# Performance work log

Measured on AMD Instinct MI355X. Metric: run time of the kernel, lower is better.

Reference implementation:

```python
import jax, jax.numpy as jnp
import numpy as np

B, T, E, H = 8, 2048, 1024, 64

def setup_inputs() -> dict:
    key = jax.random.key(0)
    k1, k2, k3, k4 = jax.random.split(key, 4)
    x = jax.random.normal(k1, (B, T, E), dtype=jnp.float32)
    # Linear(E, H, bias=False) weights stored as [E, H] (x @ W)
    s = 1.0 / np.sqrt(E)
    Wk = jax.random.normal(k2, (E, H), dtype=jnp.float32) * s
    Wq = jax.random.normal(k3, (E, H), dtype=jnp.float32) * s
    Wv = jax.random.normal(k4, (E, H), dtype=jnp.float32) * s
    return {"x": x, "Wk": Wk, "Wq": Wq, "Wv": Wv}

def reference(x, Wk, Wq, Wv):
    _, t, e = x.shape
    k = jnp.einsum('bte,eh->bth', x, Wk)
    q = jnp.einsum('bte,eh->bth', x, Wq)
    v = jnp.einsum('bte,eh->bth', x, Wv)
    # NOTE: original scales by E**-0.5 (embedding dim), not head_size**-0.5
    wei = jnp.einsum('bqh,bkh->bqk', q, k) * (e ** -0.5)
    causal = jnp.tril(jnp.ones((t, t), dtype=bool))
    wei = jnp.where(causal, wei, -jnp.inf)
    wei = jax.nn.softmax(wei, axis=-1)
    out = jnp.einsum('bqk,bkh->bqh', wei, v)
    return out
```

## Files before the change

kernel.cpp:

```cpp
#include <hip/hip_runtime.h>

typedef unsigned short u16;
typedef unsigned int u32;
typedef __bf16 bf16x8 __attribute__((ext_vector_type(8)));
typedef __bf16 bf16x4 __attribute__((ext_vector_type(4)));
typedef float f32x4 __attribute__((ext_vector_type(4)));

constexpr int Bn = 8, Tn = 2048, En = 1024, Hn = 64;
constexpr int Mrows = Bn * Tn;
constexpr float CEXP = 0.03125f * 1.4426950408889634f;

__device__ __forceinline__ u16 f2bf(float f) {
  u32 u = __float_as_uint(f);
  return (u16)((u + 0x7fffu + ((u >> 16) & 1u)) >> 16);
}

__global__ __launch_bounds__(256) void wt_kernel(
    const float* __restrict__ Wk, const float* __restrict__ Wq,
    const float* __restrict__ Wv, u16* __restrict__ Wt2) {
  __shared__ float tile[64][68];
  const int mat = blockIdx.x >> 4;
  const int tk = blockIdx.x & 15;
  const float* W = (mat == 0) ? Wk : (mat == 1) ? Wq : Wv;
  const int t = threadIdx.x;
#pragma unroll
  for (int i = 0; i < 4; ++i) {
    const int f = t + i * 256;
    const int el = f >> 4;
    const int h4 = f & 15;
    float4 v = *(const float4*)(W + (size_t)(tk * 64 + el) * Hn + h4 * 4);
    tile[el][h4 * 4 + 0] = v.x;
    tile[el][h4 * 4 + 1] = v.y;
    tile[el][h4 * 4 + 2] = v.z;
    tile[el][h4 * 4 + 3] = v.w;
  }
  __syncthreads();
#pragma unroll
  for (int c2 = 0; c2 < 2; ++c2) {
    const int c = t * 2 + c2;
    const int fi = c >> 6;
    const int l = c & 63;
    const int ht = fi >> 1, kss = fi & 1;
    const int q = l >> 4, l16 = l & 15;
    __align__(16) u16 buf[8];
#pragma unroll
    for (int j = 0; j < 8; ++j)
      buf[j] = f2bf(tile[kss * 32 + q * 8 + j][ht * 16 + l16]);
    u16* dst = Wt2 + ((size_t)(tk * 12 + mat * 4 + ht) * 2 + kss) * 512 + l * 8;
    *(uint4*)dst = *(const uint4*)buf;
  }
}

__global__ __launch_bounds__(256, 2) void qkv_kernel(
    const float* __restrict__ x, const u16* __restrict__ Wt2,
    u16* __restrict__ Kb16, u16* __restrict__ Qb16, u16* __restrict__ Vt16) {
  constexpr int NR = 32, BK = 128, LDK = BK + 8;
  __shared__ u16 xs[2][NR * LDK];
  const int t = threadIdx.x;
  const int w = t >> 6, lane = t & 63;
  const int quad = lane >> 4, l16 = lane & 15;
  const int r0 = blockIdx.x * NR;

  const int srow = t >> 5;
  const int scol = (t & 31) * 4;
  const float* xp = x + (size_t)(r0 + srow) * En + scol;

  const u16* wA = Wt2 + (size_t)lane * 8;

  f32x4 acc[3][2];
#pragma unroll
  for (int i = 0; i < 3; ++i)
#pragma unroll
    for (int nt = 0; nt < 2; ++nt) acc[i][nt] = (f32x4){0.f, 0.f, 0.f, 0.f};

  bf16x8 af[2][12];
  float4 pre[4];

#define LOADP(K0)                                                    \
  do {                                                               \
    _Pragma("unroll") for (int j_ = 0; j_ < 4; ++j_)                 \
        pre[j_] = *(const float4*)(xp + (K0) + j_ * 8 * En);         \
  } while (0)

#define LOADA(P, K0)                                                            \
  do {                                                                          \
    const int tb_ = ((K0) >> 6) * 12;                                           \
    _Pragma("unroll") for (int ks_ = 0; ks_ < 4; ++ks_)                         \
        _Pragma("unroll") for (int i_ = 0; i_ < 3; ++i_) {                      \
      const int frag_ = (tb_ + (ks_ >> 1) * 12 + (3 * w + i_)) * 2 + (ks_ & 1); \
      af[P][ks_ * 3 + i_] = *(const bf16x8*)(wA + (size_t)frag_ * 512);         \
    }                                                                           \
  } while (0)

#define WRITEX(B)                                                    \
  do {                                                               \
    u16* d_ = &xs[B][srow * LDK + scol];                             \
    _Pragma("unroll") for (int j_ = 0; j_ < 4; ++j_) {               \
      bf16x4 pk_;                                                    \
      pk_[0] = (__bf16)pre[j_].x; pk_[1] = (__bf16)pre[j_].y;        \
      pk_[2] = (__bf16)pre[j_].z; pk_[3] = (__bf16)pre[j_].w;        \
      *(bf16x4*)(d_ + j_ * 8 * LDK) = pk_;                           \
    }                                                                \
  } while (0)

#define BARRIER() asm volatile("s_waitcnt lgkmcnt(0)\ns_barrier" ::: "memory")

  LOADP(0);
  WRITEX(0);
  LOADP(BK);
  LOADA(0, 0);

#pragma unroll
  for (int s = 0; s < 8; ++s) {
    BARRIER();
    if (s < 7) WRITEX((s + 1) & 1);
    if (s < 6) LOADP((s + 2) * BK);
    if (s < 7) LOADA((s + 1) & 1, (s + 1) * BK);
    const u16* xb = &xs[s & 1][0];
#pragma unroll
    for (int ks = 0; ks < 4; ++ks) {
      bf16x8 b0 = *(const bf16x8*)(xb + l16 * LDK + ks * 32 + quad * 8);
      bf16x8 b1 = *(const bf16x8*)(xb + (16 + l16) * LDK + ks * 32 + quad * 8);
#pragma unroll
      for (int i = 0; i < 3; ++i) {
        acc[i][0] = __builtin_amdgcn_mfma_f32_16x16x32_bf16(af[s & 1][ks * 3 + i], b0, acc[i][0], 0, 0, 0);
        acc[i][1] = __builtin_amdgcn_mfma_f32_16x16x32_bf16(af[s & 1][ks * 3 + i], b1, acc[i][1], 0, 0, 0);
      }
    }
  }
#undef LOADP
#undef LOADA
#undef WRITEX
#undef BARRIER

#pragma unroll
  for (int i = 0; i < 3; ++i) {
    const int mt = 3 * w + i;
    const int mat = mt >> 2, ht = mt & 3;
#pragma unroll
    for (int nt = 0; nt < 2; ++nt) {
      const int row = r0 + nt * 16 + l16;
      f32x4 a = acc[i][nt];
      if (mat < 2) {
        u16* dst = ((mat == 0) ? Kb16 : Qb16) + (size_t)row * Hn + ht * 16 + quad * 4;
        uint2 pk;
        pk.x = (u32)f2bf(a[0]) | ((u32)f2bf(a[1]) << 16);
        pk.y = (u32)f2bf(a[2]) | ((u32)f2bf(a[3]) << 16);
        *(uint2*)dst = pk;
      } else {
        const int bb = row >> 11, tt = row & 2047;
        u16* base = Vt16 + ((size_t)bb * 64) * Tn + tt;
#pragma unroll
        for (int r = 0; r < 4; ++r)
          base[(size_t)(ht * 16 + quad * 4 + r) * Tn] = f2bf(a[r]);
      }
    }
  }
}

__global__ __launch_bounds__(512, 4) void attn_kernel(
    const u16* __restrict__ Qb16, const u16* __restrict__ Kb16,
    const u16* __restrict__ Vt16, float* __restrict__ out) {
  __shared__ __align__(16) char arena[34816];
  __shared__ float l_sh[8][32];

  u16* ptb = (u16*)arena;
  float* osb = (float*)arena;

  const int idx = blockIdx.x;
  const int b = idx & 7;
  const int tq = 63 - (idx >> 3);
  const int w = threadIdx.x >> 6, lane = threadIdx.x & 63;
  const int quad = lane >> 4, l16 = lane & 15;
  const int qbase = tq * 32;
  const int limit = qbase + 32;
  const int ch = ((limit + 255) >> 8) << 5;
  const int lo = w * ch;
  const int hi = min(lo + ch, limit);
  const int qa_abs = qbase + l16;
  const int qb_abs = qbase + 16 + l16;

  const u16* Kp = Kb16 + (size_t)b * Tn * Hn;
  const u16* Vp = Vt16 + (size_t)b * 64 * Tn;

  const u16* qrowA = Qb16 + ((size_t)b * Tn + qa_abs) * Hn + quad * 8;
  const u16* qrowB = qrowA + (size_t)16 * Hn;
  const bf16x8 qa0 = *(const bf16x8*)(qrowA);
  const bf16x8 qa1 = *(const bf16x8*)(qrowA + 32);
  const bf16x8 qb0 = *(const bf16x8*)(qrowB);
  const bf16x8 qb1 = *(const bf16x8*)(qrowB + 32);

  u16* ptw = ptb + (size_t)w * (2 * 16 * 40);

  f32x4 oA0 = {0.f, 0.f, 0.f, 0.f}, oA1 = oA0, oA2 = oA0, oA3 = oA0;
  f32x4 oB0 = oA0, oB1 = oA0, oB2 = oA0, oB3 = oA0;
  f32x4 laccA = oA0, laccB = oA0;

#pragma unroll 2
  for (int kb = lo; kb < hi; kb += 32) {
    const u16* krow0 = Kp + (size_t)(kb + l16) * Hn + quad * 8;
    const u16* krow1 = krow0 + (size_t)16 * Hn;
    const bf16x8 k0lo = *(const bf16x8*)(krow0);
    const bf16x8 k0hi = *(const bf16x8*)(krow0 + 32);
    const bf16x8 k1lo = *(const bf16x8*)(krow1);
    const bf16x8 k1hi = *(const bf16x8*)(krow1 + 32);

    const f32x4 z = {0.f, 0.f, 0.f, 0.f};
    f32x4 s0a = __builtin_amdgcn_mfma_f32_16x16x32_bf16(k0lo, qa0, z, 0, 0, 0);
    s0a = __builtin_amdgcn_mfma_f32_16x16x32_bf16(k0hi, qa1, s0a, 0, 0, 0);
    f32x4 s1a = __builtin_amdgcn_mfma_f32_16x16x32_bf16(k1lo, qa0, z, 0, 0, 0);
    s1a = __builtin_amdgcn_mfma_f32_16x16x32_bf16(k1hi, qa1, s1a, 0, 0, 0);
    f32x4 s0b = __builtin_amdgcn_mfma_f32_16x16x32_bf16(k0lo, qb0, z, 0, 0, 0);
    s0b = __builtin_amdgcn_mfma_f32_16x16x32_bf16(k0hi, qb1, s0b, 0, 0, 0);
    f32x4 s1b = __builtin_amdgcn_mfma_f32_16x16x32_bf16(k1lo, qb0, z, 0, 0, 0);
    s1b = __builtin_amdgcn_mfma_f32_16x16x32_bf16(k1hi, qb1, s1b, 0, 0, 0);

    if (kb + 15 > qbase) {
#pragma unroll
      for (int r = 0; r < 4; ++r)
        if (kb + quad * 4 + r > qa_abs) s0a[r] = -3.0e38f;
    }
    if (kb + 31 > qbase) {
#pragma unroll
      for (int r = 0; r < 4; ++r)
        if (kb + 16 + quad * 4 + r > qa_abs) s1a[r] = -3.0e38f;
    }
    if (kb + 15 > qbase + 16) {
#pragma unroll
      for (int r = 0; r < 4; ++r)
        if (kb + quad * 4 + r > qb_abs) s0b[r] = -3.0e38f;
    }
    if (kb + 31 > qbase + 16) {
#pragma unroll
      for (int r = 0; r < 4; ++r)
        if (kb + 16 + quad * 4 + r > qb_abs) s1b[r] = -3.0e38f;
    }

    f32x4 pa0, pa1, pb0v, pb1v;
#pragma unroll
    for (int r = 0; r < 4; ++r) {
      pa0[r] = __builtin_amdgcn_exp2f(s0a[r] * CEXP);
      pa1[r] = __builtin_amdgcn_exp2f(s1a[r] * CEXP);
      pb0v[r] = __builtin_amdgcn_exp2f(s0b[r] * CEXP);
      pb1v[r] = __builtin_amdgcn_exp2f(s1b[r] * CEXP);
    }
    laccA += pa0;
    laccA += pa1;
    laccB += pb0v;
    laccB += pb1v;

    {
      bf16x4 wa0, wa1, wb0, wb1;
      wa0[0] = (__bf16)pa0[0]; wa0[1] = (__bf16)pa0[1];
      wa0[2] = (__bf16)pa0[2]; wa0[3] = (__bf16)pa0[3];
      wa1[0] = (__bf16)pa1[0]; wa1[1] = (__bf16)pa1[1];
      wa1[2] = (__bf16)pa1[2]; wa1[3] = (__bf16)pa1[3];
      wb0[0] = (__bf16)pb0v[0]; wb0[1] = (__bf16)pb0v[1];
      wb0[2] = (__bf16)pb0v[2]; wb0[3] = (__bf16)pb0v[3];
      wb1[0] = (__bf16)pb1v[0]; wb1[1] = (__bf16)pb1v[1];
      wb1[2] = (__bf16)pb1v[2]; wb1[3] = (__bf16)pb1v[3];
      *(bf16x4*)&ptw[l16 * 40 + quad * 4] = wa0;
      *(bf16x4*)&ptw[l16 * 40 + 16 + quad * 4] = wa1;
      *(bf16x4*)&ptw[640 + l16 * 40 + quad * 4] = wb0;
      *(bf16x4*)&ptw[640 + l16 * 40 + 16 + quad * 4] = wb1;
    }
    const bf16x8 pba = *(const bf16x8*)&ptw[l16 * 40 + quad * 8];
    const bf16x8 pbb = *(const bf16x8*)&ptw[640 + l16 * 40 + quad * 8];

    const u16* vrow = Vp + (size_t)l16 * Tn + kb + quad * 8;
    const bf16x8 v0 = *(const bf16x8*)(vrow);
    const bf16x8 v1 = *(const bf16x8*)(vrow + (size_t)16 * Tn);
    const bf16x8 v2 = *(const bf16x8*)(vrow + (size_t)32 * Tn);
    const bf16x8 v3 = *(const bf16x8*)(vrow + (size_t)48 * Tn);

    oA0 = __builtin_amdgcn_mfma_f32_16x16x32_bf16(v0, pba, oA0, 0, 0, 0);
    oA1 = __builtin_amdgcn_mfma_f32_16x16x32_bf16(v1, pba, oA1, 0, 0, 0);
    oA2 = __builtin_amdgcn_mfma_f32_16x16x32_bf16(v2, pba, oA2, 0, 0, 0);
    oA3 = __builtin_amdgcn_mfma_f32_16x16x32_bf16(v3, pba, oA3, 0, 0, 0);
    oB0 = __builtin_amdgcn_mfma_f32_16x16x32_bf16(v0, pbb, oB0, 0, 0, 0);
    oB1 = __builtin_amdgcn_mfma_f32_16x16x32_bf16(v1, pbb, oB1, 0, 0, 0);
    oB2 = __builtin_amdgcn_mfma_f32_16x16x32_bf16(v2, pbb, oB2, 0, 0, 0);
    oB3 = __builtin_amdgcn_mfma_f32_16x16x32_bf16(v3, pbb, oB3, 0, 0, 0);
  }

  float la = (laccA[0] + laccA[1]) + (laccA[2] + laccA[3]);
  la += __shfl_xor(la, 16);
  la += __shfl_xor(la, 32);
  float lb = (laccB[0] + laccB[1]) + (laccB[2] + laccB[3]);
  lb += __shfl_xor(lb, 16);
  lb += __shfl_xor(lb, 32);
  if (quad == 0) {
    l_sh[w][l16] = la;
    l_sh[w][16 + l16] = lb;
  }
  __syncthreads();

  if (w < 4) {
    float* o0 = osb + ((size_t)w * 32 + l16) * 68;
    *(f32x4*)(o0 + 0 * 16 + quad * 4) = oA0;
    *(f32x4*)(o0 + 1 * 16 + quad * 4) = oA1;
    *(f32x4*)(o0 + 2 * 16 + quad * 4) = oA2;
    *(f32x4*)(o0 + 3 * 16 + quad * 4) = oA3;
    float* o1 = osb + ((size_t)w * 32 + 16 + l16) * 68;
    *(f32x4*)(o1 + 0 * 16 + quad * 4) = oB0;
    *(f32x4*)(o1 + 1 * 16 + quad * 4) = oB1;
    *(f32x4*)(o1 + 2 * 16 + quad * 4) = oB2;
    *(f32x4*)(o1 + 3 * 16 + quad * 4) = oB3;
  }
  __syncthreads();

  const int qq = threadIdx.x >> 4, dq = threadIdx.x & 15;
  f32x4 part = {0.f, 0.f, 0.f, 0.f};
#pragma unroll
  for (int ww = 0; ww < 4; ++ww)
    part += *(const f32x4*)&osb[((size_t)ww * 32 + qq) * 68 + dq * 4];
  __syncthreads();

  if (w >= 4) {
    float* o0 = osb + ((size_t)(w - 4) * 32 + l16) * 68;
    *(f32x4*)(o0 + 0 * 16 + quad * 4) = oA0;
    *(f32x4*)(o0 + 1 * 16 + quad * 4) = oA1;
    *(f32x4*)(o0 + 2 * 16 + quad * 4) = oA2;
    *(f32x4*)(o0 + 3 * 16 + quad * 4) = oA3;
    float* o1 = osb + ((size_t)(w - 4) * 32 + 16 + l16) * 68;
    *(f32x4*)(o1 + 0 * 16 + quad * 4) = oB0;
    *(f32x4*)(o1 + 1 * 16 + quad * 4) = oB1;
    *(f32x4*)(o1 + 2 * 16 + quad * 4) = oB2;
    *(f32x4*)(o1 + 3 * 16 + quad * 4) = oB3;
  }
  __syncthreads();

#pragma unroll
  for (int ww = 0; ww < 4; ++ww)
    part += *(const f32x4*)&osb[((size_t)ww * 32 + qq) * 68 + dq * 4];

  float lg = 0.f;
#pragma unroll
  for (int ww = 0; ww < 8; ++ww) lg += l_sh[ww][qq];
  part *= (1.f / lg);
  *(f32x4*)(out + ((size_t)b * Tn + qbase + qq) * Hn + dq * 4) = part;
}

extern "C" void kernel_launch(void* const* d_in, const int* in_sizes, int n_in,
                              void* d_out, int out_size, void* d_ws, size_t ws_size,
                              hipStream_t stream) {
  const void* x = nullptr;
  const void* Ws[3] = {nullptr, nullptr, nullptr};
  int wj = 0;
  for (int i = 0; i < n_in; ++i) {
    if (in_sizes[i] == Bn * Tn * En) x = d_in[i];
    else if (wj < 3) Ws[wj++] = d_in[i];
  }
  const float* Wk = (const float*)Ws[0];
  const float* Wq = (const float*)Ws[1];
  const float* Wv = (const float*)Ws[2];

  u16* Kb16 = (u16*)d_ws;
  u16* Qb16 = Kb16 + (size_t)Mrows * Hn;
  u16* Vt16 = Qb16 + (size_t)Mrows * Hn;
  u16* Wt2  = Vt16 + (size_t)Mrows * Hn;

  wt_kernel<<<48, 256, 0, stream>>>(Wk, Wq, Wv, Wt2);
  qkv_kernel<<<Mrows / 32, 256, 0, stream>>>((const float*)x, Wt2, Kb16, Qb16, Vt16);
  attn_kernel<<<Bn * (Tn / 32), 512, 0, stream>>>(Qb16, Kb16, Vt16, (float*)d_out);
}
```

Measured before the change: 133.3 us.

## Split QKV projection K-dimension across two wave groups with LDS reduction

The QKV projection kernel goes from 256 to 512 threads per block. The two halves of the waves each handle half of every 128-wide K chunk, and the partial accumulators are combined through a shared-memory reduction before the bf16 outputs are written. Each thread now loads half as much x data and half as many weight fragments, which cuts register pressure and raises occupancy (launch bounds 512,4) so the memory-bound x stream has more latency hiding. In exchange it adds a 24 KB LDS reduction buffer, an extra barrier, and an idle phase for half the waves at the end.

Measured after the change: 130.7 us. 1.02x faster.

```diff
diff --git a/kernel.cpp b/kernel.cpp
--- a/kernel.cpp
+++ b/kernel.cpp
@@ -51,18 +51,21 @@
   }
 }
 
-__global__ __launch_bounds__(256, 2) void qkv_kernel(
+__global__ __launch_bounds__(512, 4) void qkv_kernel(
     const float* __restrict__ x, const u16* __restrict__ Wt2,
     u16* __restrict__ Kb16, u16* __restrict__ Qb16, u16* __restrict__ Vt16) {
   constexpr int NR = 32, BK = 128, LDK = BK + 8;
   __shared__ u16 xs[2][NR * LDK];
+  __shared__ __align__(16) float red[6][4][64][4];
   const int t = threadIdx.x;
   const int w = t >> 6, lane = t & 63;
   const int quad = lane >> 4, l16 = lane & 15;
+  const int wl = w & 3;
+  const int wh = w >> 2;
   const int r0 = blockIdx.x * NR;
 
-  const int srow = t >> 5;
-  const int scol = (t & 31) * 4;
+  const int srow = t >> 4;
+  const int scol = (t & 15) * 8;
   const float* xp = x + (size_t)(r0 + srow) * En + scol;
 
   const u16* wA = Wt2 + (size_t)lane * 8;
@@ -73,34 +76,34 @@
 #pragma unroll
     for (int nt = 0; nt < 2; ++nt) acc[i][nt] = (f32x4){0.f, 0.f, 0.f, 0.f};
 
-  bf16x8 af[2][12];
-  float4 pre[4];
-
-#define LOADP(K0)                                                    \
-  do {                                                               \
-    _Pragma("unroll") for (int j_ = 0; j_ < 4; ++j_)                 \
-        pre[j_] = *(const float4*)(xp + (K0) + j_ * 8 * En);         \
+  bf16x8 af[2][6];
+  float4 pre[2];
+
+#define LOADP(K0)                                  \
+  do {                                             \
+    pre[0] = *(const float4*)(xp + (K0));          \
+    pre[1] = *(const float4*)(xp + (K0) + 4);      \
   } while (0)
 
-#define LOADA(P, K0)                                                            \
-  do {                                                                          \
-    const int tb_ = ((K0) >> 6) * 12;                                           \
-    _Pragma("unroll") for (int ks_ = 0; ks_ < 4; ++ks_)                         \
-        _Pragma("unroll") for (int i_ = 0; i_ < 3; ++i_) {                      \
-      const int frag_ = (tb_ + (ks_ >> 1) * 12 + (3 * w + i_)) * 2 + (ks_ & 1); \
-      af[P][ks_ * 3 + i_] = *(const bf16x8*)(wA + (size_t)frag_ * 512);         \
-    }                                                                           \
+#define LOADA(P, K0)                                                          \
+  do {                                                                        \
+    const int tb_ = ((K0) >> 6) * 12;                                         \
+    _Pragma("unroll") for (int ks_ = 0; ks_ < 2; ++ks_)                       \
+        _Pragma("unroll") for (int i_ = 0; i_ < 3; ++i_) {                    \
+      const int frag_ = (tb_ + wh * 12 + (3 * wl + i_)) * 2 + ks_;            \
+      af[P][ks_ * 3 + i_] = *(const bf16x8*)(wA + (size_t)frag_ * 512);       \
+    }                                                                         \
   } while (0)
 
-#define WRITEX(B)                                                    \
-  do {                                                               \
-    u16* d_ = &xs[B][srow * LDK + scol];                             \
-    _Pragma("unroll") for (int j_ = 0; j_ < 4; ++j_) {               \
-      bf16x4 pk_;                                                    \
-      pk_[0] = (__bf16)pre[j_].x; pk_[1] = (__bf16)pre[j_].y;        \
-      pk_[2] = (__bf16)pre[j_].z; pk_[3] = (__bf16)pre[j_].w;        \
-      *(bf16x4*)(d_ + j_ * 8 * LDK) = pk_;                           \
-    }                                                                \
+#define WRITEX(B)                                                  \
+  do {                                                             \
+    u16* d_ = &xs[B][srow * LDK + scol];                           \
+    bf16x8 pk_;                                                    \
+    pk_[0] = (__bf16)pre[0].x; pk_[1] = (__bf16)pre[0].y;          \
+    pk_[2] = (__bf16)pre[0].z; pk_[3] = (__bf16)pre[0].w;          \
+    pk_[4] = (__bf16)pre[1].x; pk_[5] = (__bf16)pre[1].y;          \
+    pk_[6] = (__bf16)pre[1].z; pk_[7] = (__bf16)pre[1].w;          \
+    *(bf16x8*)d_ = pk_;                                            \
   } while (0)
 
 #define BARRIER() asm volatile("s_waitcnt lgkmcnt(0)\ns_barrier" ::: "memory")
@@ -116,9 +119,9 @@
     if (s < 7) WRITEX((s + 1) & 1);
     if (s < 6) LOADP((s + 2) * BK);
     if (s < 7) LOADA((s + 1) & 1, (s + 1) * BK);
-    const u16* xb = &xs[s & 1][0];
-#pragma unroll
-    for (int ks = 0; ks < 4; ++ks) {
+    const u16* xb = &xs[s & 1][0] + wh * 64;
+#pragma unroll
+    for (int ks = 0; ks < 2; ++ks) {
       bf16x8 b0 = *(const bf16x8*)(xb + l16 * LDK + ks * 32 + quad * 8);
       bf16x8 b1 = *(const bf16x8*)(xb + (16 + l16) * LDK + ks * 32 + quad * 8);
 #pragma unroll
@@ -133,26 +136,36 @@
 #undef WRITEX
 #undef BARRIER
 
-#pragma unroll
-  for (int i = 0; i < 3; ++i) {
-    const int mt = 3 * w + i;
-    const int mat = mt >> 2, ht = mt & 3;
-#pragma unroll
-    for (int nt = 0; nt < 2; ++nt) {
-      const int row = r0 + nt * 16 + l16;
-      f32x4 a = acc[i][nt];
-      if (mat < 2) {
-        u16* dst = ((mat == 0) ? Kb16 : Qb16) + (size_t)row * Hn + ht * 16 + quad * 4;
-        uint2 pk;
-        pk.x = (u32)f2bf(a[0]) | ((u32)f2bf(a[1]) << 16);
-        pk.y = (u32)f2bf(a[2]) | ((u32)f2bf(a[3]) << 16);
-        *(uint2*)dst = pk;
-      } else {
-        const int bb = row >> 11, tt = row & 2047;
-        u16* base = Vt16 + ((size_t)bb * 64) * Tn + tt;
-#pragma unroll
-        for (int r = 0; r < 4; ++r)
-          base[(size_t)(ht * 16 + quad * 4 + r) * Tn] = f2bf(a[r]);
+  if (w >= 4) {
+#pragma unroll
+    for (int i = 0; i < 3; ++i)
+#pragma unroll
+      for (int nt = 0; nt < 2; ++nt)
+        *(f32x4*)&red[i * 2 + nt][w - 4][lane][0] = acc[i][nt];
+  }
+  __syncthreads();
+  if (w < 4) {
+#pragma unroll
+    for (int i = 0; i < 3; ++i) {
+      const int mt = 3 * wl + i;
+      const int mat = mt >> 2, ht = mt & 3;
+#pragma unroll
+      for (int nt = 0; nt < 2; ++nt) {
+        const int row = r0 + nt * 16 + l16;
+        f32x4 a = acc[i][nt] + *(const f32x4*)&red[i * 2 + nt][w][lane][0];
+        if (mat < 2) {
+          u16* dst = ((mat == 0) ? Kb16 : Qb16) + (size_t)row * Hn + ht * 16 + quad * 4;
+          uint2 pk;
+          pk.x = (u32)f2bf(a[0]) | ((u32)f2bf(a[1]) << 16);
+          pk.y = (u32)f2bf(a[2]) | ((u32)f2bf(a[3]) << 16);
+          *(uint2*)dst = pk;
+        } else {
+          const int bb = row >> 11, tt = row & 2047;
+          u16* base = Vt16 + ((size_t)bb * 64) * Tn + tt;
+#pragma unroll
+          for (int r = 0; r < 4; ++r)
+            base[(size_t)(ht * 16 + quad * 4 + r) * Tn] = f2bf(a[r]);
+        }
       }
     }
   }
@@ -361,6 +374,6 @@
   u16* Wt2  = Vt16 + (size_t)Mrows * Hn;
 
   wt_kernel<<<48, 256, 0, stream>>>(Wk, Wq, Wv, Wt2);
-  qkv_kernel<<<Mrows / 32, 256, 0, stream>>>((const float*)x, Wt2, Kb16, Qb16, Vt16);
+  qkv_kernel<<<Mrows / 32, 512, 0, stream>>>((const float*)x, Wt2, Kb16, Qb16, Vt16);
   attn_kernel<<<Bn * (Tn / 32), 512, 0, stream>>>(Qb16, Kb16, Vt16, (float*)d_out);
 }
```
